# Optimization experiments

Hardware: AMD Instinct MI355X
Metric: run time of the kernel (lower is better)

The kernel has to match this reference:

```python
import jax, jax.numpy as jnp
import numpy as np

VOCAB, D, B, S, L, K = 50000, 256, 128, 64, 32, 32
EPS = 1e-12  # tf.nn.l2_normalize epsilon


def setup_inputs() -> dict:
    key = jax.random.key(0)
    ks = jax.random.split(key, 7)
    prgrph = jax.random.randint(ks[0], (B, S, L), 0, VOCAB, dtype=jnp.int32)
    prgrph_mask = jax.random.randint(ks[1], (B, S, L), 0, 2, dtype=jnp.int32).astype(bool)
    keys = jax.random.normal(ks[2], (B, K, D), dtype=jnp.float32)
    embedding_matrix = jax.random.normal(ks[3], (VOCAB, D), dtype=jnp.float32) * 0.05
    U = jax.random.normal(ks[4], (D, D), dtype=jnp.float32) * 0.05
    V = jax.random.normal(ks[5], (D, D), dtype=jnp.float32) * 0.05
    W = jax.random.normal(ks[6], (D, D), dtype=jnp.float32) * 0.05
    return {"prgrph": prgrph, "prgrph_mask": prgrph_mask, "keys": keys,
            "embedding_matrix": embedding_matrix, "U": U, "V": V, "W": W}


def reference(prgrph, prgrph_mask, keys, embedding_matrix, U, V, W):
    # bag-of-words sentence encoding: [B, S, L, D] -> sum over words -> [B, S, D]
    enc_sents = embedding_matrix[prgrph].sum(axis=2)
    sent_mask = prgrph_mask[:, :, 0]  # [B, S] sentence availability

    h0 = jnp.zeros_like(keys)  # initial entity hidden state [B, K, D]

    def step(h, inp):
        e, m = inp  # e: [B, D], m: [B] bool
        # gate_i = sigmoid(sum_d e * (h_i + k_i))  -> [B, K]
        gate = jax.nn.sigmoid(jnp.einsum('bd,bkd->bk', e, h + keys))
        # h_tilda = relu(h U + k V + e W)  -> [B, K, D]
        h_tilda = jax.nn.relu(
            jnp.einsum('bkd,de->bke', h, U)
            + jnp.einsum('bkd,de->bke', keys, V)
            + (e @ W)[:, None, :]
        )
        upd = h + gate[..., None] * h_tilda
        upd = upd * jax.lax.rsqrt(jnp.maximum((upd * upd).sum(-1, keepdims=True), EPS))
        h_new = jnp.where(m[:, None, None], upd, h)  # masked rows keep prev state
        return h_new, None

    h_final, _ = jax.lax.scan(step, h0, (enc_sents.transpose(1, 0, 2), sent_mask.T))
    return h_final  # [B, K, D]
```

## Files before the change

### kernel.cpp

```cpp
#include <hip/hip_runtime.h>

#define D 256
#define B 128
#define S 64
#define L 32
#define K 32
#define KH 16
#define NW 8
#define NSUB 2
#define HSTR 260

typedef _Float16 f16x8 __attribute__((ext_vector_type(8)));
typedef float f32x4 __attribute__((ext_vector_type(4)));
typedef unsigned short u16;

__device__ __forceinline__ u16 h_bits(_Float16 h) {
    union { _Float16 h; u16 u; } x; x.h = h; return x.u;
}

__global__ __launch_bounds__(256) void pre_kernel(
    const int* __restrict__ prgrph, const float* __restrict__ E,
    const float* __restrict__ Wm, const float* __restrict__ Vm,
    const float* __restrict__ keys, const void* __restrict__ mraw,
    float* __restrict__ enc, float* __restrict__ eW,
    float* __restrict__ keysV, float* __restrict__ ek,
    int* __restrict__ mask_out) {
    const int t = threadIdx.x, wave = t >> 6, lane = t & 63;
    __shared__ int   flag;
    __shared__ int   smask[32];
    __shared__ int   sidx[32][L];
    __shared__ float a_s[32][264];
    __shared__ float ks[32][260];

    const float* Bm;
    float* O;

    if (blockIdx.x < (B * S) / 32) {
        const int bid = blockIdx.x;

        if (t == 0) flag = 0;
        __syncthreads();
        {
            const unsigned int* w32 = (const unsigned int*)mraw;
            int loc = 0;
            #pragma unroll
            for (int j = 0; j < 4; ++j)
                if (w32[t * 4 + j] > 1u) loc = 1;
            if (loc) flag = 1;
        }
        #pragma unroll
        for (int j = 0; j < 4; ++j) {
            const int idx = t * 4 + j;
            sidx[idx >> 5][idx & 31] = prgrph[(size_t)bid * 1024 + idx];
        }
        __syncthreads();
        if (t < 32) {
            const int gi = bid * 32 + t;
            const int mv = (flag != 0)
                ? (int)((const unsigned char*)mraw)[(size_t)gi * L]
                : ((const int*)mraw)[(size_t)gi * L];
            smask[t] = mv;
            mask_out[gi] = mv;
        }
        __syncthreads();

        const float4* E4 = (const float4*)E;
        for (int sl = wave * 8; sl < wave * 8 + 8; ++sl) {
            if (!smask[sl]) continue;
            float4 a = make_float4(0.f, 0.f, 0.f, 0.f);
            #pragma unroll
            for (int l = 0; l < L; ++l) {
                const float4 v = E4[(size_t)sidx[sl][l] * (D / 4) + lane];
                a.x += v.x; a.y += v.y; a.z += v.z; a.w += v.w;
            }
            *(float4*)&a_s[sl][lane * 4] = a;
            *(float4*)&enc[(size_t)(bid * 32 + sl) * D + lane * 4] = a;
        }
        __syncthreads();
        Bm = Wm;
        O = eW + (size_t)bid * 32 * D;
    } else {
        const int row0 = (blockIdx.x - (B * S) / 32) * 32;
        const float4* Ag = (const float4*)(keys + (size_t)row0 * D);
        for (int i = t; i < 32 * D / 4; i += 256) {
            const float4 v = Ag[i];
            *(float4*)&a_s[i >> 6][(i & 63) * 4] = v;
        }
        __syncthreads();
        Bm = Vm;
        O = keysV + (size_t)row0 * D;
    }

    {
        const int r0 = wave * 8, c0 = lane * 4;
        float4 acc[8];
        #pragma unroll
        for (int i = 0; i < 8; ++i) acc[i] = make_float4(0.f, 0.f, 0.f, 0.f);
        for (int d = 0; d < D; d += 4) {
            float4 av[8];
            #pragma unroll
            for (int i = 0; i < 8; ++i) av[i] = *(const float4*)&a_s[r0 + i][d];
            #pragma unroll
            for (int j = 0; j < 4; ++j) {
                const float4 w = *(const float4*)(Bm + (size_t)(d + j) * D + c0);
                #pragma unroll
                for (int i = 0; i < 8; ++i) {
                    const float a = (j == 0) ? av[i].x : (j == 1) ? av[i].y
                                  : (j == 2) ? av[i].z : av[i].w;
                    acc[i].x += a * w.x; acc[i].y += a * w.y;
                    acc[i].z += a * w.z; acc[i].w += a * w.w;
                }
            }
        }
        #pragma unroll
        for (int i = 0; i < 8; ++i)
            *(float4*)&O[(size_t)(r0 + i) * D + c0] = acc[i];
    }

    if (blockIdx.x >= (B * S) / 32) return;

    {
        const int bid = blockIdx.x;
        const int b = bid >> 1;
        const float4* kg = (const float4*)(keys + (size_t)b * K * D);
        for (int i = t; i < K * D / 4; i += 256) {
            const float4 v = kg[i];
            *(float4*)&ks[i >> 6][(i & 63) * 4] = v;
        }
        __syncthreads();
        const int sl = t >> 3, kq = t & 7;
        if (smask[sl]) {
            float acc[4];
            #pragma unroll
            for (int j = 0; j < 4; ++j) acc[j] = 0.f;
            for (int d4 = 0; d4 < D / 4; ++d4) {
                const float4 e = *(const float4*)&a_s[sl][d4 * 4];
                #pragma unroll
                for (int j = 0; j < 4; ++j) {
                    const float4 kv = *(const float4*)&ks[kq + 8 * j][d4 * 4];
                    acc[j] += e.x * kv.x + e.y * kv.y + e.z * kv.z + e.w * kv.w;
                }
            }
            #pragma unroll
            for (int j = 0; j < 4; ++j)
                ek[(size_t)(bid * 32 + sl) * K + kq + 8 * j] = acc[j];
        }
    }
}

__global__ __launch_bounds__(512, 2) void recur_kernel(
    const float* __restrict__ enc, const float* __restrict__ eWp,
    const float* __restrict__ keysV, const float* __restrict__ ek,
    const float* __restrict__ U, const int* __restrict__ mask,
    float* __restrict__ out) {
    const int b  = blockIdx.x >> 1;
    const int kh = (blockIdx.x & 1) * KH;
    const int t = threadIdx.x;
    const int wave = t >> 6, lane = t & 63;
    const int n = lane & 15, quad = lane >> 4;
    const int col2 = wave * 32 + 2 * n;

    __shared__ u16 hF[2][KH][HSTR];
    __shared__ float redN[2][KH][NW];
    __shared__ float redG[2][KH][NW];

    f16x8 Uhi[NSUB][8], Ulo[NSUB][8];
    #pragma unroll
    for (int sub = 0; sub < NSUB; ++sub) {
        const int col = col2 + sub;
        #pragma unroll
        for (int kt = 0; kt < 8; ++kt) {
            #pragma unroll
            for (int j = 0; j < 8; ++j) {
                const int k = kt * 32 + quad * 8 + j;
                const float u = U[(size_t)k * D + col];
                const _Float16 uh = (_Float16)u;
                Uhi[sub][kt][j] = uh;
                Ulo[sub][kt][j] = (_Float16)(u - (float)uh);
            }
        }
    }
    #pragma unroll
    for (int sub = 0; sub < NSUB; ++sub)
        #pragma unroll
        for (int kt = 0; kt < 8; ++kt)
            asm volatile("" : "+a"(Uhi[sub][kt]), "+a"(Ulo[sub][kt]));

    float upv[4][NSUB];
    float rn[4];
    float keysVc[4][NSUB];
    #pragma unroll
    for (int reg = 0; reg < 4; ++reg) {
        rn[reg] = 1.f;
        const size_t base = (size_t)(b * K + kh + quad * 4 + reg) * D;
        const float2 kv2 = *(const float2*)&keysV[base + col2];
        keysVc[reg][0] = kv2.x; keysVc[reg][1] = kv2.y;
        upv[reg][0] = 0.f; upv[reg][1] = 0.f;
    }

    const int* bm = mask + b * S;
    unsigned long long rem = __ballot(bm[lane & 63] != 0);

    float eWc[NSUB];
    float4 ekv = make_float4(0.f, 0.f, 0.f, 0.f);
    eWc[0] = 0.f; eWc[1] = 0.f;
    if (rem) {
        const int s0 = (int)__builtin_ctzll(rem);
        const float2 w2 = *(const float2*)&eWp[(size_t)(b * S + s0) * D + col2];
        eWc[0] = w2.x; eWc[1] = w2.y;
        ekv = *(const float4*)(ek + (size_t)(b * S + s0) * K + kh + quad * 4);
    }

    int p = 0, q = 0;
    bool first = true;
    while (rem) {
        rem &= rem - 1;
        const int sn = rem ? (int)__builtin_ctzll(rem) : -1;

        float e_n[NSUB];
        e_n[0] = 0.f; e_n[1] = 0.f;
        if (sn >= 0) {
            const float2 e2 = *(const float2*)&enc[(size_t)(b * S + sn) * D + col2];
            e_n[0] = e2.x; e_n[1] = e2.y;
        }

        f32x4 acc[NSUB][2];
        #pragma unroll
        for (int sub = 0; sub < NSUB; ++sub) {
            acc[sub][0] = (f32x4){0.f, 0.f, 0.f, 0.f};
            acc[sub][1] = (f32x4){0.f, 0.f, 0.f, 0.f};
        }
        if (!first) {
            #pragma unroll
            for (int kt = 0; kt < 8; ++kt) {
                const f16x8 av = *(const f16x8*)&hF[p][n][kt * 32 + quad * 8];
                #pragma unroll
                for (int sub = 0; sub < NSUB; ++sub) {
                    acc[sub][0] = __builtin_amdgcn_mfma_f32_16x16x32_f16(av, Uhi[sub][kt], acc[sub][0], 0, 0, 0);
                    acc[sub][1] = __builtin_amdgcn_mfma_f32_16x16x32_f16(av, Ulo[sub][kt], acc[sub][1], 0, 0, 0);
                }
            }
        }

        float gate[4];
        #pragma unroll
        for (int reg = 0; reg < 4; ++reg) {
            const float ekb = (reg == 0) ? ekv.x : (reg == 1) ? ekv.y
                            : (reg == 2) ? ekv.z : ekv.w;
            float g = ekb;
            if (!first) {
                const float* rg = redG[q ^ 1][quad * 4 + reg];
                const float4 g0 = *(const float4*)rg;
                const float4 g1 = *(const float4*)(rg + 4);
                g += rn[reg] * (g0.x + g0.y + g0.z + g0.w +
                                g1.x + g1.y + g1.z + g1.w);
            }
            gate[reg] = 1.f / (1.f + __expf(-g));
        }

        const int pw = p ^ 1;
        float pn[4], gd[4];
        #pragma unroll
        for (int reg = 0; reg < 4; ++reg) {
            const int row = quad * 4 + reg;
            float sq = 0.f, dv = 0.f;
            float u2s[2];
            #pragma unroll
            for (int sub = 0; sub < NSUB; ++sub) {
                const float asum = acc[sub][0][reg] + acc[sub][1][reg];
                float ht = rn[reg] * asum + keysVc[reg][sub] + eWc[sub];
                ht = fmaxf(ht, 0.f);
                const float u2 = rn[reg] * upv[reg][sub] + gate[reg] * ht;
                upv[reg][sub] = u2;
                u2s[sub] = u2;
                sq += u2 * u2;
                dv += u2 * e_n[sub];
            }
            const unsigned int packed =
                ((unsigned int)h_bits((_Float16)u2s[1]) << 16) |
                (unsigned int)h_bits((_Float16)u2s[0]);
            *(unsigned int*)&hF[pw][row][col2] = packed;
            pn[reg] = sq;
            gd[reg] = dv;
        }

        if (sn >= 0) {
            const float2 w2 = *(const float2*)&eWp[(size_t)(b * S + sn) * D + col2];
            eWc[0] = w2.x; eWc[1] = w2.y;
            ekv = *(const float4*)(ek + (size_t)(b * S + sn) * K + kh + quad * 4);
        }

        {
            float v0 = pn[0], v1 = pn[1], v2 = pn[2], v3 = pn[3];
            float w0 = gd[0], w1 = gd[1], w2 = gd[2], w3 = gd[3];
            {
                const bool hi = (n & 1);
                float k0 = hi ? w0 : v0, x0 = hi ? v0 : w0;
                float k1 = hi ? w1 : v1, x1 = hi ? v1 : w1;
                float k2 = hi ? w2 : v2, x2 = hi ? v2 : w2;
                float k3 = hi ? w3 : v3, x3 = hi ? v3 : w3;
                v0 = k0 + __shfl_xor(x0, 1);
                v1 = k1 + __shfl_xor(x1, 1);
                v2 = k2 + __shfl_xor(x2, 1);
                v3 = k3 + __shfl_xor(x3, 1);
            }
            {
                const bool hi = (n & 2);
                float k0 = hi ? v2 : v0, x0 = hi ? v0 : v2;
                float k1 = hi ? v3 : v1, x1 = hi ? v1 : v3;
                v0 = k0 + __shfl_xor(x0, 2);
                v1 = k1 + __shfl_xor(x1, 2);
            }
            {
                const bool hi = (n & 4);
                float k0 = hi ? v1 : v0, x0 = hi ? v0 : v1;
                v0 = k0 + __shfl_xor(x0, 4);
            }
            v0 += __shfl_xor(v0, 8);
            if (n < 8) {
                const int vid = ((n & 1) << 2) | (n & 2) | ((n >> 2) & 1);
                const int row = quad * 4 + (vid & 3);
                float* dst = (vid & 4) ? &redG[q][row][wave]
                                       : &redN[q][row][wave];
                *dst = v0;
            }
        }

        __syncthreads();

        #pragma unroll
        for (int reg = 0; reg < 4; ++reg) {
            const float* rp = redN[q][quad * 4 + reg];
            const float4 r0 = *(const float4*)rp;
            const float4 r1 = *(const float4*)(rp + 4);
            rn[reg] = rsqrtf(fmaxf(r0.x + r0.y + r0.z + r0.w +
                                   r1.x + r1.y + r1.z + r1.w, 1e-12f));
        }
        p ^= 1; q ^= 1; first = false;
    }

    #pragma unroll
    for (int reg = 0; reg < 4; ++reg) {
        const size_t base = (size_t)(b * K + kh + quad * 4 + reg) * D;
        const float2 o2 = make_float2(rn[reg] * upv[reg][0],
                                      rn[reg] * upv[reg][1]);
        *(float2*)&out[base + col2] = o2;
    }
}

extern "C" void kernel_launch(void* const* d_in, const int* in_sizes, int n_in,
                              void* d_out, int out_size, void* d_ws, size_t ws_size,
                              hipStream_t stream) {
    const int*   prgrph = (const int*)d_in[0];
    const void*  pmask  = d_in[1];
    const float* keys   = (const float*)d_in[2];
    const float* E      = (const float*)d_in[3];
    const float* U      = (const float*)d_in[4];
    const float* V      = (const float*)d_in[5];
    const float* W      = (const float*)d_in[6];
    float* out = (float*)d_out;

    float* ws_enc   = (float*)d_ws;
    float* ws_eW    = ws_enc + (size_t)B * S * D;
    float* ws_keysV = ws_eW  + (size_t)B * S * D;
    float* ws_ek    = ws_keysV + (size_t)B * K * D;
    int*   ws_mask  = (int*)(ws_ek + (size_t)B * S * K);

    pre_kernel<<<(B * S) / 32 + (B * K) / 32, 256, 0, stream>>>(
        prgrph, E, W, V, keys, pmask, ws_enc, ws_eW, ws_keysV, ws_ek, ws_mask);
    recur_kernel<<<B * (K / KH), 512, 0, stream>>>(
        ws_enc, ws_eW, ws_keysV, ws_ek, U, ws_mask, out);
}
```

Baseline: 216.0 us.

## Fuse precompute into recurrence kernel with MFMA projections kept in LDS

Merges the separate pre-kernel into the recurrence kernel. Each block now gathers its batch's bag-of-words sums and computes eW, e·k and keys·V with split-fp16 MFMA, storing eW (as fp16) and e·k in shared memory instead of global workspace. This removes a kernel launch and the global round trips for the intermediates. In exchange, the gather and projections are done twice per batch because both K-half blocks repeat them. It also uses much more LDS, the fp16 storage of eW loses precision, and blocks that read another block's enc_g writes could race.

```diff
diff --git a/kernel.cpp b/kernel.cpp
--- a/kernel.cpp
+++ b/kernel.cpp
@@ -13,146 +13,21 @@
 typedef _Float16 f16x8 __attribute__((ext_vector_type(8)));
 typedef float f32x4 __attribute__((ext_vector_type(4)));
 typedef unsigned short u16;
+typedef unsigned int u32;
 
 __device__ __forceinline__ u16 h_bits(_Float16 h) {
     union { _Float16 h; u16 u; } x; x.h = h; return x.u;
 }
-
-__global__ __launch_bounds__(256) void pre_kernel(
+__device__ __forceinline__ _Float16 f16_bits(u16 v) {
+    union { u16 u; _Float16 h; } x; x.u = v; return x.h;
+}
+
+__global__ __launch_bounds__(512, 2) void fused_kernel(
     const int* __restrict__ prgrph, const float* __restrict__ E,
     const float* __restrict__ Wm, const float* __restrict__ Vm,
     const float* __restrict__ keys, const void* __restrict__ mraw,
-    float* __restrict__ enc, float* __restrict__ eW,
-    float* __restrict__ keysV, float* __restrict__ ek,
-    int* __restrict__ mask_out) {
-    const int t = threadIdx.x, wave = t >> 6, lane = t & 63;
-    __shared__ int   flag;
-    __shared__ int   smask[32];
-    __shared__ int   sidx[32][L];
-    __shared__ float a_s[32][264];
-    __shared__ float ks[32][260];
-
-    const float* Bm;
-    float* O;
-
-    if (blockIdx.x < (B * S) / 32) {
-        const int bid = blockIdx.x;
-
-        if (t == 0) flag = 0;
-        __syncthreads();
-        {
-            const unsigned int* w32 = (const unsigned int*)mraw;
-            int loc = 0;
-            #pragma unroll
-            for (int j = 0; j < 4; ++j)
-                if (w32[t * 4 + j] > 1u) loc = 1;
-            if (loc) flag = 1;
-        }
-        #pragma unroll
-        for (int j = 0; j < 4; ++j) {
-            const int idx = t * 4 + j;
-            sidx[idx >> 5][idx & 31] = prgrph[(size_t)bid * 1024 + idx];
-        }
-        __syncthreads();
-        if (t < 32) {
-            const int gi = bid * 32 + t;
-            const int mv = (flag != 0)
-                ? (int)((const unsigned char*)mraw)[(size_t)gi * L]
-                : ((const int*)mraw)[(size_t)gi * L];
-            smask[t] = mv;
-            mask_out[gi] = mv;
-        }
-        __syncthreads();
-
-        const float4* E4 = (const float4*)E;
-        for (int sl = wave * 8; sl < wave * 8 + 8; ++sl) {
-            if (!smask[sl]) continue;
-            float4 a = make_float4(0.f, 0.f, 0.f, 0.f);
-            #pragma unroll
-            for (int l = 0; l < L; ++l) {
-                const float4 v = E4[(size_t)sidx[sl][l] * (D / 4) + lane];
-                a.x += v.x; a.y += v.y; a.z += v.z; a.w += v.w;
-            }
-            *(float4*)&a_s[sl][lane * 4] = a;
-            *(float4*)&enc[(size_t)(bid * 32 + sl) * D + lane * 4] = a;
-        }
-        __syncthreads();
-        Bm = Wm;
-        O = eW + (size_t)bid * 32 * D;
-    } else {
-        const int row0 = (blockIdx.x - (B * S) / 32) * 32;
-        const float4* Ag = (const float4*)(keys + (size_t)row0 * D);
-        for (int i = t; i < 32 * D / 4; i += 256) {
-            const float4 v = Ag[i];
-            *(float4*)&a_s[i >> 6][(i & 63) * 4] = v;
-        }
-        __syncthreads();
-        Bm = Vm;
-        O = keysV + (size_t)row0 * D;
-    }
-
-    {
-        const int r0 = wave * 8, c0 = lane * 4;
-        float4 acc[8];
-        #pragma unroll
-        for (int i = 0; i < 8; ++i) acc[i] = make_float4(0.f, 0.f, 0.f, 0.f);
-        for (int d = 0; d < D; d += 4) {
-            float4 av[8];
-            #pragma unroll
-            for (int i = 0; i < 8; ++i) av[i] = *(const float4*)&a_s[r0 + i][d];
-            #pragma unroll
-            for (int j = 0; j < 4; ++j) {
-                const float4 w = *(const float4*)(Bm + (size_t)(d + j) * D + c0);
-                #pragma unroll
-                for (int i = 0; i < 8; ++i) {
-                    const float a = (j == 0) ? av[i].x : (j == 1) ? av[i].y
-                                  : (j == 2) ? av[i].z : av[i].w;
-                    acc[i].x += a * w.x; acc[i].y += a * w.y;
-                    acc[i].z += a * w.z; acc[i].w += a * w.w;
-                }
-            }
-        }
-        #pragma unroll
-        for (int i = 0; i < 8; ++i)
-            *(float4*)&O[(size_t)(r0 + i) * D + c0] = acc[i];
-    }
-
-    if (blockIdx.x >= (B * S) / 32) return;
-
-    {
-        const int bid = blockIdx.x;
-        const int b = bid >> 1;
-        const float4* kg = (const float4*)(keys + (size_t)b * K * D);
-        for (int i = t; i < K * D / 4; i += 256) {
-            const float4 v = kg[i];
-            *(float4*)&ks[i >> 6][(i & 63) * 4] = v;
-        }
-        __syncthreads();
-        const int sl = t >> 3, kq = t & 7;
-        if (smask[sl]) {
-            float acc[4];
-            #pragma unroll
-            for (int j = 0; j < 4; ++j) acc[j] = 0.f;
-            for (int d4 = 0; d4 < D / 4; ++d4) {
-                const float4 e = *(const float4*)&a_s[sl][d4 * 4];
-                #pragma unroll
-                for (int j = 0; j < 4; ++j) {
-                    const float4 kv = *(const float4*)&ks[kq + 8 * j][d4 * 4];
-                    acc[j] += e.x * kv.x + e.y * kv.y + e.z * kv.z + e.w * kv.w;
-                }
-            }
-            #pragma unroll
-            for (int j = 0; j < 4; ++j)
-                ek[(size_t)(bid * 32 + sl) * K + kq + 8 * j] = acc[j];
-        }
-    }
-}
-
-__global__ __launch_bounds__(512, 2) void recur_kernel(
-    const float* __restrict__ enc, const float* __restrict__ eWp,
-    const float* __restrict__ keysV, const float* __restrict__ ek,
-    const float* __restrict__ U, const int* __restrict__ mask,
-    float* __restrict__ out) {
+    const float* __restrict__ U,
+    float* __restrict__ enc_g, float* __restrict__ out) {
     const int b  = blockIdx.x >> 1;
     const int kh = (blockIdx.x & 1) * KH;
     const int t = threadIdx.x;
@@ -160,9 +35,182 @@
     const int n = lane & 15, quad = lane >> 4;
     const int col2 = wave * 32 + 2 * n;
 
-    __shared__ u16 hF[2][KH][HSTR];
+    __shared__ u16   hF[2][KH][HSTR];
     __shared__ float redN[2][KH][NW];
     __shared__ float redG[2][KH][NW];
+    __shared__ u16   eWh[S][260];
+    __shared__ float ekl[S][20];
+    __shared__ int   smask[S];
+    __shared__ int   flag;
+    int* sidx = (int*)&hF[0][0][0];
+
+    if (t == 0) flag = 0;
+    __syncthreads();
+    {
+        const u32* w32 = (const u32*)mraw;
+        int loc = 0;
+        #pragma unroll
+        for (int j = 0; j < 2; ++j)
+            if (w32[t * 2 + j] > 1u) loc = 1;
+        if (loc) flag = 1;
+    }
+    #pragma unroll
+    for (int j = 0; j < 4; ++j) {
+        const int idx = t * 4 + j;
+        sidx[idx] = prgrph[(size_t)b * (S * L) + idx];
+    }
+    __syncthreads();
+    if (t < S) {
+        const size_t gi = (size_t)(b * S + t) * L;
+        smask[t] = (flag != 0) ? (int)((const unsigned char*)mraw)[gi]
+                               : ((const int*)mraw)[gi];
+    }
+    __syncthreads();
+
+    {
+        const float4* E4 = (const float4*)E;
+        for (int sl = wave * 8; sl < wave * 8 + 8; ++sl) {
+            if (!smask[sl]) continue;
+            float4 a = make_float4(0.f, 0.f, 0.f, 0.f);
+            #pragma unroll
+            for (int l = 0; l < L; ++l) {
+                const float4 v = E4[(size_t)sidx[sl * L + l] * (D / 4) + lane];
+                a.x += v.x; a.y += v.y; a.z += v.z; a.w += v.w;
+            }
+            *(float4*)&enc_g[(size_t)(b * S + sl) * D + lane * 4] = a;
+        }
+    }
+    __syncthreads();
+
+    f16x8 Kh[8], Kl[8];
+    #pragma unroll
+    for (int kt = 0; kt < 8; ++kt) {
+        #pragma unroll
+        for (int j = 0; j < 8; ++j) {
+            const float v = keys[(size_t)(b * K + kh + n) * D + kt * 32 + quad * 8 + j];
+            const _Float16 vh = (_Float16)v;
+            Kh[kt][j] = vh;
+            Kl[kt][j] = (_Float16)(v - (float)vh);
+        }
+    }
+
+    {
+        f16x8 Bh[NSUB][8], Bl[NSUB][8];
+        #pragma unroll
+        for (int sub = 0; sub < NSUB; ++sub) {
+            const int col = col2 + sub;
+            #pragma unroll
+            for (int kt = 0; kt < 8; ++kt) {
+                #pragma unroll
+                for (int j = 0; j < 8; ++j) {
+                    const float w = Wm[(size_t)(kt * 32 + quad * 8 + j) * D + col];
+                    const _Float16 wh = (_Float16)w;
+                    Bh[sub][kt][j] = wh;
+                    Bl[sub][kt][j] = (_Float16)(w - (float)wh);
+                }
+            }
+        }
+        #pragma unroll
+        for (int tile = 0; tile < 4; ++tile) {
+            f32x4 acc[NSUB];
+            acc[0] = (f32x4){0.f, 0.f, 0.f, 0.f};
+            acc[1] = (f32x4){0.f, 0.f, 0.f, 0.f};
+            #pragma unroll
+            for (int kt = 0; kt < 8; ++kt) {
+                const float* ep = enc_g + (size_t)(b * S + tile * 16 + n) * D
+                                + kt * 32 + quad * 8;
+                const float4 e0 = *(const float4*)ep;
+                const float4 e1 = *(const float4*)(ep + 4);
+                f16x8 ah, al;
+                #pragma unroll
+                for (int j = 0; j < 8; ++j) {
+                    const float v = (j < 4) ? ((const float*)&e0)[j]
+                                            : ((const float*)&e1)[j - 4];
+                    const _Float16 vh = (_Float16)v;
+                    ah[j] = vh;
+                    al[j] = (_Float16)(v - (float)vh);
+                }
+                #pragma unroll
+                for (int sub = 0; sub < NSUB; ++sub) {
+                    acc[sub] = __builtin_amdgcn_mfma_f32_16x16x32_f16(ah, Bh[sub][kt], acc[sub], 0, 0, 0);
+                    acc[sub] = __builtin_amdgcn_mfma_f32_16x16x32_f16(ah, Bl[sub][kt], acc[sub], 0, 0, 0);
+                    acc[sub] = __builtin_amdgcn_mfma_f32_16x16x32_f16(al, Bh[sub][kt], acc[sub], 0, 0, 0);
+                }
+            }
+            #pragma unroll
+            for (int reg = 0; reg < 4; ++reg) {
+                const u32 packed =
+                    ((u32)h_bits((_Float16)acc[1][reg]) << 16) |
+                    (u32)h_bits((_Float16)acc[0][reg]);
+                *(u32*)&eWh[tile * 16 + quad * 4 + reg][col2] = packed;
+            }
+        }
+    }
+
+    #pragma unroll
+    for (int tile = 0; tile < 4; ++tile) {
+        f32x4 acc = (f32x4){0.f, 0.f, 0.f, 0.f};
+        #pragma unroll
+        for (int kt = 0; kt < 8; ++kt) {
+            const float* ep = enc_g + (size_t)(b * S + tile * 16 + n) * D
+                            + kt * 32 + quad * 8;
+            const float4 e0 = *(const float4*)ep;
+            const float4 e1 = *(const float4*)(ep + 4);
+            f16x8 ah, al;
+            #pragma unroll
+            for (int j = 0; j < 8; ++j) {
+                const float v = (j < 4) ? ((const float*)&e0)[j]
+                                        : ((const float*)&e1)[j - 4];
+                const _Float16 vh = (_Float16)v;
+                ah[j] = vh;
+                al[j] = (_Float16)(v - (float)vh);
+            }
+            acc = __builtin_amdgcn_mfma_f32_16x16x32_f16(ah, Kh[kt], acc, 0, 0, 0);
+            acc = __builtin_amdgcn_mfma_f32_16x16x32_f16(ah, Kl[kt], acc, 0, 0, 0);
+            acc = __builtin_amdgcn_mfma_f32_16x16x32_f16(al, Kh[kt], acc, 0, 0, 0);
+        }
+        #pragma unroll
+        for (int reg = 0; reg < 4; ++reg)
+            ekl[tile * 16 + quad * 4 + reg][n] = acc[reg];
+    }
+
+    float keysVc[4][NSUB];
+    {
+        f16x8 Vh[NSUB][8], Vl[NSUB][8];
+        #pragma unroll
+        for (int sub = 0; sub < NSUB; ++sub) {
+            const int col = col2 + sub;
+            #pragma unroll
+            for (int kt = 0; kt < 8; ++kt) {
+                #pragma unroll
+                for (int j = 0; j < 8; ++j) {
+                    const float v = Vm[(size_t)(kt * 32 + quad * 8 + j) * D + col];
+                    const _Float16 vh = (_Float16)v;
+                    Vh[sub][kt][j] = vh;
+                    Vl[sub][kt][j] = (_Float16)(v - (float)vh);
+                }
+            }
+        }
+        f32x4 accV[NSUB];
+        accV[0] = (f32x4){0.f, 0.f, 0.f, 0.f};
+        accV[1] = (f32x4){0.f, 0.f, 0.f, 0.f};
+        #pragma unroll
+        for (int kt = 0; kt < 8; ++kt) {
+            #pragma unroll
+            for (int sub = 0; sub < NSUB; ++sub) {
+                accV[sub] = __builtin_amdgcn_mfma_f32_16x16x32_f16(Kh[kt], Vh[sub][kt], accV[sub], 0, 0, 0);
+                accV[sub] = __builtin_amdgcn_mfma_f32_16x16x32_f16(Kh[kt], Vl[sub][kt], accV[sub], 0, 0, 0);
+                accV[sub] = __builtin_amdgcn_mfma_f32_16x16x32_f16(Kl[kt], Vh[sub][kt], accV[sub], 0, 0, 0);
+            }
+        }
+        #pragma unroll
+        for (int reg = 0; reg < 4; ++reg) {
+            keysVc[reg][0] = accV[0][reg];
+            keysVc[reg][1] = accV[1][reg];
+        }
+    }
+
+    __syncthreads();
 
     f16x8 Uhi[NSUB][8], Ulo[NSUB][8];
     #pragma unroll
@@ -188,27 +236,23 @@
 
     float upv[4][NSUB];
     float rn[4];
-    float keysVc[4][NSUB];
     #pragma unroll
     for (int reg = 0; reg < 4; ++reg) {
         rn[reg] = 1.f;
-        const size_t base = (size_t)(b * K + kh + quad * 4 + reg) * D;
-        const float2 kv2 = *(const float2*)&keysV[base + col2];
-        keysVc[reg][0] = kv2.x; keysVc[reg][1] = kv2.y;
         upv[reg][0] = 0.f; upv[reg][1] = 0.f;
     }
 
-    const int* bm = mask + b * S;
-    unsigned long long rem = __ballot(bm[lane & 63] != 0);
+    unsigned long long rem = __ballot(smask[lane] != 0);
 
     float eWc[NSUB];
     float4 ekv = make_float4(0.f, 0.f, 0.f, 0.f);
     eWc[0] = 0.f; eWc[1] = 0.f;
     if (rem) {
         const int s0 = (int)__builtin_ctzll(rem);
-        const float2 w2 = *(const float2*)&eWp[(size_t)(b * S + s0) * D + col2];
-        eWc[0] = w2.x; eWc[1] = w2.y;
-        ekv = *(const float4*)(ek + (size_t)(b * S + s0) * K + kh + quad * 4);
+        const u32 w = *(const u32*)&eWh[s0][col2];
+        eWc[0] = (float)f16_bits((u16)(w & 0xffff));
+        eWc[1] = (float)f16_bits((u16)(w >> 16));
+        ekv = *(const float4*)&ekl[s0][quad * 4];
     }
 
     int p = 0, q = 0;
@@ -220,7 +264,7 @@
         float e_n[NSUB];
         e_n[0] = 0.f; e_n[1] = 0.f;
         if (sn >= 0) {
-            const float2 e2 = *(const float2*)&enc[(size_t)(b * S + sn) * D + col2];
+            const float2 e2 = *(const float2*)&enc_g[(size_t)(b * S + sn) * D + col2];
             e_n[0] = e2.x; e_n[1] = e2.y;
         }
 
@@ -276,18 +320,19 @@
                 sq += u2 * u2;
                 dv += u2 * e_n[sub];
             }
-            const unsigned int packed =
-                ((unsigned int)h_bits((_Float16)u2s[1]) << 16) |
-                (unsigned int)h_bits((_Float16)u2s[0]);
-            *(unsigned int*)&hF[pw][row][col2] = packed;
+            const u32 packed =
+                ((u32)h_bits((_Float16)u2s[1]) << 16) |
+                (u32)h_bits((_Float16)u2s[0]);
+            *(u32*)&hF[pw][row][col2] = packed;
             pn[reg] = sq;
             gd[reg] = dv;
         }
 
         if (sn >= 0) {
-            const float2 w2 = *(const float2*)&eWp[(size_t)(b * S + sn) * D + col2];
-            eWc[0] = w2.x; eWc[1] = w2.y;
-            ekv = *(const float4*)(ek + (size_t)(b * S + sn) * K + kh + quad * 4);
+            const u32 w = *(const u32*)&eWh[sn][col2];
+            eWc[0] = (float)f16_bits((u16)(w & 0xffff));
+            eWc[1] = (float)f16_bits((u16)(w >> 16));
+            ekv = *(const float4*)&ekl[sn][quad * 4];
         }
 
         {
@@ -360,14 +405,8 @@
     const float* W      = (const float*)d_in[6];
     float* out = (float*)d_out;
 
-    float* ws_enc   = (float*)d_ws;
-    float* ws_eW    = ws_enc + (size_t)B * S * D;
-    float* ws_keysV = ws_eW  + (size_t)B * S * D;
-    float* ws_ek    = ws_keysV + (size_t)B * K * D;
-    int*   ws_mask  = (int*)(ws_ek + (size_t)B * S * K);
-
-    pre_kernel<<<(B * S) / 32 + (B * K) / 32, 256, 0, stream>>>(
-        prgrph, E, W, V, keys, pmask, ws_enc, ws_eW, ws_keysV, ws_ek, ws_mask);
-    recur_kernel<<<B * (K / KH), 512, 0, stream>>>(
-        ws_enc, ws_eW, ws_keysV, ws_ek, U, ws_mask, out);
+    float* ws_enc = (float*)d_ws;
+
+    fused_kernel<<<B * (K / KH), 512, 0, stream>>>(
+        prgrph, E, W, V, keys, pmask, U, ws_enc, out);
 }
```

After: 299.3 us. 38.6% more time.

## Use split-fp16 MFMA for eW, keysV and ek projections in pre_kernel

Applied to the files above, without the earlier changes.

The three fp32 FMA projections in pre_kernel (enc·W, keys·V, enc·keysᵀ) become MFMA 16x16x32 f16 ops. Each fp32 operand is split into a high and a low fp16 part, and three MFMAs per tile keep near-fp32 accuracy. Blocks now cover 16 rows instead of 32, so twice as many blocks launch, and LDS staging of the A tiles is dropped in favour of reading enc back from global memory. In exchange, B is read with strided scalar loads and converted in every block. The low-by-low product is skipped, and masked-out rows are fed in uninitialized.

```diff
diff --git a/kernel.cpp b/kernel.cpp
--- a/kernel.cpp
+++ b/kernel.cpp
@@ -13,9 +13,30 @@
 typedef _Float16 f16x8 __attribute__((ext_vector_type(8)));
 typedef float f32x4 __attribute__((ext_vector_type(4)));
 typedef unsigned short u16;
+typedef unsigned int u32;
 
 __device__ __forceinline__ u16 h_bits(_Float16 h) {
     union { _Float16 h; u16 u; } x; x.h = h; return x.u;
+}
+__device__ __forceinline__ void cvt8(const float* p, f16x8& hi, f16x8& lo) {
+    const float4 a = *(const float4*)p;
+    const float4 b = *(const float4*)(p + 4);
+    #pragma unroll
+    for (int j = 0; j < 8; ++j) {
+        const float v = (j < 4) ? ((const float*)&a)[j] : ((const float*)&b)[j - 4];
+        const _Float16 vh = (_Float16)v;
+        hi[j] = vh;
+        lo[j] = (_Float16)(v - (float)vh);
+    }
+}
+__device__ __forceinline__ void cvt8s(const float* p, f16x8& hi, f16x8& lo) {
+    #pragma unroll
+    for (int j = 0; j < 8; ++j) {
+        const float v = p[(size_t)j * D];
+        const _Float16 vh = (_Float16)v;
+        hi[j] = vh;
+        lo[j] = (_Float16)(v - (float)vh);
+    }
 }
 
 __global__ __launch_bounds__(256) void pre_kernel(
@@ -26,22 +47,18 @@
     float* __restrict__ keysV, float* __restrict__ ek,
     int* __restrict__ mask_out) {
     const int t = threadIdx.x, wave = t >> 6, lane = t & 63;
-    __shared__ int   flag;
-    __shared__ int   smask[32];
-    __shared__ int   sidx[32][L];
-    __shared__ float a_s[32][264];
-    __shared__ float ks[32][260];
-
-    const float* Bm;
-    float* O;
-
-    if (blockIdx.x < (B * S) / 32) {
+    const int n = lane & 15, quad = lane >> 4;
+
+    if (blockIdx.x < (B * S) / 16) {
         const int bid = blockIdx.x;
-
+        const int b = bid >> 2;
+        __shared__ int flag;
+        __shared__ int smask[16];
+        __shared__ int sidx[16][L];
         if (t == 0) flag = 0;
         __syncthreads();
         {
-            const unsigned int* w32 = (const unsigned int*)mraw;
+            const u32* w32 = (const u32*)mraw;
             int loc = 0;
             #pragma unroll
             for (int j = 0; j < 4; ++j)
@@ -49,13 +66,13 @@
             if (loc) flag = 1;
         }
         #pragma unroll
-        for (int j = 0; j < 4; ++j) {
-            const int idx = t * 4 + j;
-            sidx[idx >> 5][idx & 31] = prgrph[(size_t)bid * 1024 + idx];
-        }
-        __syncthreads();
-        if (t < 32) {
-            const int gi = bid * 32 + t;
+        for (int j = 0; j < 2; ++j) {
+            const int idx = t * 2 + j;
+            sidx[idx >> 5][idx & 31] = prgrph[(size_t)bid * (16 * L) + idx];
+        }
+        __syncthreads();
+        if (t < 16) {
+            const int gi = bid * 16 + t;
             const int mv = (flag != 0)
                 ? (int)((const unsigned char*)mraw)[(size_t)gi * L]
                 : ((const int*)mraw)[(size_t)gi * L];
@@ -64,86 +81,78 @@
         }
         __syncthreads();
 
-        const float4* E4 = (const float4*)E;
-        for (int sl = wave * 8; sl < wave * 8 + 8; ++sl) {
-            if (!smask[sl]) continue;
-            float4 a = make_float4(0.f, 0.f, 0.f, 0.f);
-            #pragma unroll
-            for (int l = 0; l < L; ++l) {
-                const float4 v = E4[(size_t)sidx[sl][l] * (D / 4) + lane];
-                a.x += v.x; a.y += v.y; a.z += v.z; a.w += v.w;
-            }
-            *(float4*)&a_s[sl][lane * 4] = a;
-            *(float4*)&enc[(size_t)(bid * 32 + sl) * D + lane * 4] = a;
-        }
-        __syncthreads();
-        Bm = Wm;
-        O = eW + (size_t)bid * 32 * D;
+        {
+            const float4* E4 = (const float4*)E;
+            for (int sl = wave * 4; sl < wave * 4 + 4; ++sl) {
+                if (!smask[sl]) continue;
+                float4 a = make_float4(0.f, 0.f, 0.f, 0.f);
+                #pragma unroll
+                for (int l = 0; l < L; ++l) {
+                    const float4 v = E4[(size_t)sidx[sl][l] * (D / 4) + lane];
+                    a.x += v.x; a.y += v.y; a.z += v.z; a.w += v.w;
+                }
+                *(float4*)&enc[(size_t)(bid * 16 + sl) * D + lane * 4] = a;
+            }
+        }
+        __syncthreads();
+
+        f16x8 ah[8], al[8];
+        #pragma unroll
+        for (int kt = 0; kt < 8; ++kt)
+            cvt8(enc + (size_t)(bid * 16 + n) * D + kt * 32 + quad * 8,
+                 ah[kt], al[kt]);
+
+        #pragma unroll
+        for (int sub = 0; sub < 4; ++sub) {
+            const int col = wave * 64 + sub * 16 + n;
+            f32x4 acc = (f32x4){0.f, 0.f, 0.f, 0.f};
+            for (int kt = 0; kt < 8; ++kt) {
+                f16x8 bh, bl;
+                cvt8s(Wm + (size_t)(kt * 32 + quad * 8) * D + col, bh, bl);
+                acc = __builtin_amdgcn_mfma_f32_16x16x32_f16(ah[kt], bh, acc, 0, 0, 0);
+                acc = __builtin_amdgcn_mfma_f32_16x16x32_f16(ah[kt], bl, acc, 0, 0, 0);
+                acc = __builtin_amdgcn_mfma_f32_16x16x32_f16(al[kt], bh, acc, 0, 0, 0);
+            }
+            #pragma unroll
+            for (int reg = 0; reg < 4; ++reg)
+                eW[(size_t)(bid * 16 + quad * 4 + reg) * D + col] = acc[reg];
+        }
+
+        if (wave < 2) {
+            const int ent = wave * 16 + n;
+            f32x4 acc = (f32x4){0.f, 0.f, 0.f, 0.f};
+            for (int kt = 0; kt < 8; ++kt) {
+                f16x8 kh, kl;
+                cvt8(keys + (size_t)(b * K + ent) * D + kt * 32 + quad * 8, kh, kl);
+                acc = __builtin_amdgcn_mfma_f32_16x16x32_f16(ah[kt], kh, acc, 0, 0, 0);
+                acc = __builtin_amdgcn_mfma_f32_16x16x32_f16(ah[kt], kl, acc, 0, 0, 0);
+                acc = __builtin_amdgcn_mfma_f32_16x16x32_f16(al[kt], kh, acc, 0, 0, 0);
+            }
+            #pragma unroll
+            for (int reg = 0; reg < 4; ++reg)
+                ek[(size_t)(bid * 16 + quad * 4 + reg) * K + ent] = acc[reg];
+        }
     } else {
-        const int row0 = (blockIdx.x - (B * S) / 32) * 32;
-        const float4* Ag = (const float4*)(keys + (size_t)row0 * D);
-        for (int i = t; i < 32 * D / 4; i += 256) {
-            const float4 v = Ag[i];
-            *(float4*)&a_s[i >> 6][(i & 63) * 4] = v;
-        }
-        __syncthreads();
-        Bm = Vm;
-        O = keysV + (size_t)row0 * D;
-    }
-
-    {
-        const int r0 = wave * 8, c0 = lane * 4;
-        float4 acc[8];
-        #pragma unroll
-        for (int i = 0; i < 8; ++i) acc[i] = make_float4(0.f, 0.f, 0.f, 0.f);
-        for (int d = 0; d < D; d += 4) {
-            float4 av[8];
-            #pragma unroll
-            for (int i = 0; i < 8; ++i) av[i] = *(const float4*)&a_s[r0 + i][d];
-            #pragma unroll
-            for (int j = 0; j < 4; ++j) {
-                const float4 w = *(const float4*)(Bm + (size_t)(d + j) * D + c0);
-                #pragma unroll
-                for (int i = 0; i < 8; ++i) {
-                    const float a = (j == 0) ? av[i].x : (j == 1) ? av[i].y
-                                  : (j == 2) ? av[i].z : av[i].w;
-                    acc[i].x += a * w.x; acc[i].y += a * w.y;
-                    acc[i].z += a * w.z; acc[i].w += a * w.w;
-                }
-            }
-        }
-        #pragma unroll
-        for (int i = 0; i < 8; ++i)
-            *(float4*)&O[(size_t)(r0 + i) * D + c0] = acc[i];
-    }
-
-    if (blockIdx.x >= (B * S) / 32) return;
-
-    {
-        const int bid = blockIdx.x;
-        const int b = bid >> 1;
-        const float4* kg = (const float4*)(keys + (size_t)b * K * D);
-        for (int i = t; i < K * D / 4; i += 256) {
-            const float4 v = kg[i];
-            *(float4*)&ks[i >> 6][(i & 63) * 4] = v;
-        }
-        __syncthreads();
-        const int sl = t >> 3, kq = t & 7;
-        if (smask[sl]) {
-            float acc[4];
-            #pragma unroll
-            for (int j = 0; j < 4; ++j) acc[j] = 0.f;
-            for (int d4 = 0; d4 < D / 4; ++d4) {
-                const float4 e = *(const float4*)&a_s[sl][d4 * 4];
-                #pragma unroll
-                for (int j = 0; j < 4; ++j) {
-                    const float4 kv = *(const float4*)&ks[kq + 8 * j][d4 * 4];
-                    acc[j] += e.x * kv.x + e.y * kv.y + e.z * kv.z + e.w * kv.w;
-                }
-            }
-            #pragma unroll
-            for (int j = 0; j < 4; ++j)
-                ek[(size_t)(bid * 32 + sl) * K + kq + 8 * j] = acc[j];
+        const int idx = blockIdx.x - (B * S) / 16;
+        f16x8 ah[8], al[8];
+        #pragma unroll
+        for (int kt = 0; kt < 8; ++kt)
+            cvt8(keys + (size_t)(idx * 16 + n) * D + kt * 32 + quad * 8,
+                 ah[kt], al[kt]);
+        #pragma unroll
+        for (int sub = 0; sub < 4; ++sub) {
+            const int col = wave * 64 + sub * 16 + n;
+            f32x4 acc = (f32x4){0.f, 0.f, 0.f, 0.f};
+            for (int kt = 0; kt < 8; ++kt) {
+                f16x8 bh, bl;
+                cvt8s(Vm + (size_t)(kt * 32 + quad * 8) * D + col, bh, bl);
+                acc = __builtin_amdgcn_mfma_f32_16x16x32_f16(ah[kt], bh, acc, 0, 0, 0);
+                acc = __builtin_amdgcn_mfma_f32_16x16x32_f16(ah[kt], bl, acc, 0, 0, 0);
+                acc = __builtin_amdgcn_mfma_f32_16x16x32_f16(al[kt], bh, acc, 0, 0, 0);
+            }
+            #pragma unroll
+            for (int reg = 0; reg < 4; ++reg)
+                keysV[(size_t)(idx * 16 + quad * 4 + reg) * D + col] = acc[reg];
         }
     }
 }
@@ -199,7 +208,7 @@
     }
 
     const int* bm = mask + b * S;
-    unsigned long long rem = __ballot(bm[lane & 63] != 0);
+    unsigned long long rem = __ballot(bm[lane] != 0);
 
     float eWc[NSUB];
     float4 ekv = make_float4(0.f, 0.f, 0.f, 0.f);
@@ -276,10 +285,10 @@
                 sq += u2 * u2;
                 dv += u2 * e_n[sub];
             }
-            const unsigned int packed =
-                ((unsigned int)h_bits((_Float16)u2s[1]) << 16) |
-                (unsigned int)h_bits((_Float16)u2s[0]);
-            *(unsigned int*)&hF[pw][row][col2] = packed;
+            const u32 packed =
+                ((u32)h_bits((_Float16)u2s[1]) << 16) |
+                (u32)h_bits((_Float16)u2s[0]);
+            *(u32*)&hF[pw][row][col2] = packed;
             pn[reg] = sq;
             gd[reg] = dv;
         }
@@ -366,7 +375,7 @@
     float* ws_ek    = ws_keysV + (size_t)B * K * D;
     int*   ws_mask  = (int*)(ws_ek + (size_t)B * S * K);
 
-    pre_kernel<<<(B * S) / 32 + (B * K) / 32, 256, 0, stream>>>(
+    pre_kernel<<<(B * S) / 16 + (B * K) / 16, 256, 0, stream>>>(
         prgrph, E, W, V, keys, pmask, ws_enc, ws_eW, ws_keysV, ws_ek, ws_mask);
     recur_kernel<<<B * (K / KH), 512, 0, stream>>>(
         ws_enc, ws_eW, ws_keysV, ws_ek, U, ws_mask, out);
```

Result: slower. 733.3 us (+239.5%).
